# Performance work log

Hardware: AMD Instinct MI355X
Metric: run time of the kernel (lower is better)

The kernel has to match this reference:

```python
import jax, jax.numpy as jnp
import numpy as np

COORD_DIM, PARAM_DIM, H, L, O = 3, 8, 128, 5, 5
B, N_PTS = 16, 50000


def setup_inputs() -> dict:
    key = jax.random.key(0)
    ks = jax.random.split(key, 16)
    def w(k, shape, fan_in):
        return jax.random.normal(k, shape, dtype=jnp.float32) / np.sqrt(fan_in)
    inp = {
        "coords": jax.random.normal(ks[0], (B, N_PTS, COORD_DIM), dtype=jnp.float32),
        "params": jax.random.normal(ks[1], (B, PARAM_DIM), dtype=jnp.float32),
        # branch MLP: param_dim -> H (x5 hidden, rowdy tanh) -> H*O
        "branch_W0": w(ks[2], (PARAM_DIM, H), PARAM_DIM),
        "branch_b0": jnp.zeros((H,), jnp.float32),
        "branch_Wh": w(ks[3], (L - 1, H, H), H),
        "branch_bh": jnp.zeros((L - 1, H), jnp.float32),
        "branch_alpha": jnp.ones((L, H), jnp.float32),
        "branch_Wf": w(ks[4], (H, H * O), H),
        "branch_bf": jnp.zeros((H * O,), jnp.float32),
        # trunk: coord_dim -> H (x5, FiLM by branch cumsum, rowdy tanh) -> H
        "trunk_W0": w(ks[5], (COORD_DIM, H), COORD_DIM),
        "trunk_b0": jnp.zeros((H,), jnp.float32),
        "trunk_Wh": w(ks[6], (L - 1, H, H), H),
        "trunk_bh": jnp.zeros((L - 1, H), jnp.float32),
        "trunk_alpha": jnp.ones((L, H), jnp.float32),
        "trunk_Wf": w(ks[7], (H, H), H),
        "trunk_bf": jnp.zeros((H,), jnp.float32),
    }
    return inp


def reference(coords, params, branch_W0, branch_b0, branch_Wh, branch_bh,
              branch_alpha, branch_Wf, branch_bf, trunk_W0, trunk_b0,
              trunk_Wh, trunk_bh, trunk_alpha, trunk_Wf, trunk_bf):
    # ---- branch MLP with RowdyActivation, keeping hidden outputs ----
    h = branch_alpha[0] * jnp.tanh(params @ branch_W0 + branch_b0)  # (B,H)
    hiddens = [h]
    for i in range(L - 1):
        h = branch_alpha[i + 1] * jnp.tanh(h @ branch_Wh[i] + branch_bh[i])
        hiddens.append(h)
    branch_out = h @ branch_Wf + branch_bf  # (B, H*O)
    # cumulative sums S_i = sum_{j<=i} hidden_j
    S = [hiddens[0]]
    for i in range(1, L):
        S.append(hiddens[i] + S[-1])
    # ---- trunk with FiLM modulation ----
    x = coords @ trunk_W0 + trunk_b0                       # (B,n,H)
    x = trunk_alpha[0] * jnp.tanh(x * S[0][:, None, :])
    for i in range(1, L):
        x = x @ trunk_Wh[i - 1] + trunk_bh[i - 1]
        x = trunk_alpha[i] * jnp.tanh(x * S[i][:, None, :])
    YL = x @ trunk_Wf + trunk_bf                           # (B,n,H)
    ZL = branch_out.reshape(B, O, H)                       # (B,O,H)
    # out[b,n,o] = sum_h ZL[b,o,h] * YL[b,n,h]  (tiled matmul, no (B,n,O,H) temp)
    return jnp.einsum('bnh,boh->bno', YL, ZL)
```

## Files before the change

kernel.cpp:

```cpp
#include <hip/hip_runtime.h>
#include <math.h>

#define H      128
#define LNUM   5
#define ONUM   5
#define BATCH  16
#define NPTS   50000
#define TP     64
#define XROW   152

#define K2LOG2E 2.8853900817779268f

typedef _Float16      half8    __attribute__((ext_vector_type(8)));
typedef float         floatx4  __attribute__((ext_vector_type(4)));
typedef unsigned int  uint2v   __attribute__((ext_vector_type(2)));
typedef unsigned int  uint4v   __attribute__((ext_vector_type(4)));
typedef unsigned short ushort8_t __attribute__((ext_vector_type(8)));

#define BAR() asm volatile("s_waitcnt lgkmcnt(0)\ns_barrier" ::: "memory")

static __device__ __forceinline__ unsigned short f2h(float f) {
    _Float16 h = (_Float16)f;
    return __builtin_bit_cast(unsigned short, h);
}
static __device__ __forceinline__ unsigned int packh(float a, float b) {
    return (unsigned int)f2h(a) | ((unsigned int)f2h(b) << 16);
}

__global__ __launch_bounds__(512)
void fold_kernel(const float* __restrict__ params,
                 const float* __restrict__ bW0, const float* __restrict__ bb0,
                 const float* __restrict__ bWh, const float* __restrict__ bbh,
                 const float* __restrict__ balpha,
                 const float* __restrict__ bWf, const float* __restrict__ bbf,
                 const float* __restrict__ tW0, const float* __restrict__ tb0,
                 const float* __restrict__ tWh, const float* __restrict__ tbh,
                 const float* __restrict__ tWf, const float* __restrict__ talpha,
                 const float* __restrict__ tbf,
                 unsigned short* __restrict__ w0s, unsigned short* __restrict__ whs,
                 unsigned short* __restrict__ wcomb, float* __restrict__ bcomb,
                 float* __restrict__ binit) {
    const int b = blockIdx.x, l = blockIdx.y, t = threadIdx.x;
    __shared__ float hbuf[H];
    __shared__ float Sneed[H];
    __shared__ float pbuf[8];
    __shared__ float zl_sh[ONUM][H];
    if (t < 8) pbuf[t] = params[b * 8 + t];
    __syncthreads();

    float scum = 0.0f;
    if (t < H) {
        float acc = bb0[t];
        for (int k = 0; k < 8; ++k) acc += pbuf[k] * bW0[k * H + t];
        float h = balpha[t] * tanhf(acc);
        hbuf[t] = h;
        scum = h;
        if (l == 0) Sneed[t] = scum;
    }
    for (int i = 1; i < LNUM; ++i) {
        __syncthreads();
        float hn = 0.0f;
        if (t < H) {
            const float* Wl = bWh + (i - 1) * H * H;
            float a2 = bbh[(i - 1) * H + t];
            for (int k = 0; k < H; ++k) a2 += hbuf[k] * Wl[k * H + t];
            hn = balpha[i * H + t] * tanhf(a2);
        }
        __syncthreads();
        if (t < H) {
            hbuf[t] = hn;
            scum += hn;
            if (i == l) Sneed[t] = scum;
        }
    }
    __syncthreads();

    if (l == 5) {
        for (int idx = t; idx < ONUM * H; idx += 512) {
            int o = idx >> 7, hh = idx & 127;
            float z = bbf[o * H + hh];
            for (int k = 0; k < H; ++k) z += hbuf[k] * bWf[k * (H * ONUM) + o * H + hh];
            zl_sh[o][hh] = z;
        }
        __syncthreads();
        for (int j = t; j < 16 * H; j += 512) {
            int o = j >> 7, f = j & 127;
            float v = 0.0f;
            if (o < ONUM) {
                const float* wfr = tWf + f * H;
                float s = 0.0f;
                for (int h = 0; h < H; ++h) s += wfr[h] * zl_sh[o][h];
                v = talpha[4 * H + f] * s;
            }
            wcomb[b * 16 * H + j] = f2h(v);
        }
        if (t < 16) {
            float v = 0.0f;
            if (t < ONUM)
                for (int h = 0; h < H; ++h) v += tbf[h] * zl_sh[t][h];
            bcomb[b * 16 + t] = v;
        }
    } else if (l == 0) {
        if (t < H) binit[(b * LNUM + 0) * H + t] = K2LOG2E * Sneed[t] * tb0[t];
        unsigned int* dst = (unsigned int*)(w0s + b * H * 32);
        for (int j = t; j < H * 16; j += 512) {
            int f = j >> 4, k0 = (j & 15) << 1;
            float s = K2LOG2E * Sneed[f];
            float v0 = (k0 < 3)     ? s * tW0[k0 * H + f]       : 0.0f;
            float v1 = (k0 + 1 < 3) ? s * tW0[(k0 + 1) * H + f] : 0.0f;
            dst[j] = packh(v0, v1);
        }
    } else {
        if (t < H) binit[(b * LNUM + l) * H + t] = K2LOG2E * Sneed[t] * tbh[(l - 1) * H + t];
        const float* Wsrc = tWh + (l - 1) * H * H;
        unsigned int* dst = (unsigned int*)(whs + (b * 4 + (l - 1)) * H * H);
        for (int j = t; j < H * H / 2; j += 512) {
            int f = j >> 6, k0 = (j & 63) << 1;
            float s = K2LOG2E * Sneed[f];
            dst[j] = packh(s * Wsrc[k0 * H + f] * talpha[(l - 1) * H + k0],
                           s * Wsrc[(k0 + 1) * H + f] * talpha[(l - 1) * H + k0 + 1]);
        }
    }
}

__global__ __launch_bounds__(128, 3)
void trunk_kernel(const float* __restrict__ coords,
                  const unsigned short* __restrict__ w0s,
                  const unsigned short* __restrict__ whs,
                  const float* __restrict__ binit,
                  const unsigned short* __restrict__ wcomb,
                  const float* __restrict__ bcomb,
                  float* __restrict__ out) {
    const int b    = blockIdx.y;
    const int n0   = blockIdx.x * TP;
    const int tid  = threadIdx.x;
    const int lane = tid & 63;
    const int w    = tid >> 6;
    const int q    = lane >> 4;
    const int c    = lane & 15;
    const int mh   = w * 64;

    __shared__ unsigned short xs[TP * XROW];

    int valid = NPTS - n0; if (valid > TP) valid = TP;
    {
        int p = tid >> 1, hh = tid & 1;
        if (hh == 0) {
            float c0 = 0.f, c1 = 0.f, c2 = 0.f;
            if (p < valid) {
                const float* cp = coords + ((size_t)b * NPTS + n0 + p) * 3;
                c0 = cp[0]; c1 = cp[1]; c2 = cp[2];
            }
            uint4v z;
            z.x = __builtin_bit_cast(unsigned int, __builtin_amdgcn_cvt_pkrtz(c0, c1));
            z.y = __builtin_bit_cast(unsigned int, __builtin_amdgcn_cvt_pkrtz(c2, 0.0f));
            z.z = 0; z.w = 0;
            *(uint4v*)&xs[p * XROW + 0] = z;
            uint4v zz = {0, 0, 0, 0};
            *(uint4v*)&xs[p * XROW + 8] = zz;
        } else {
            uint4v zz = {0, 0, 0, 0};
            *(uint4v*)&xs[p * XROW + 16] = zz;
            *(uint4v*)&xs[p * XROW + 24] = zz;
        }
    }
    BAR();

    floatx4 acc[4][4];

    #pragma unroll
    for (int mt = 0; mt < 4; ++mt) {
        floatx4 bi4 = *(const floatx4*)&binit[(b * LNUM + 0) * H + mh + mt * 16 + q * 4];
        #pragma unroll
        for (int nt = 0; nt < 4; ++nt) acc[mt][nt] = bi4;
    }
    {
        const unsigned short* w0b = w0s + b * H * 32;
        half8 af[4], bfr[4];
        #pragma unroll
        for (int mt = 0; mt < 4; ++mt)
            af[mt] = __builtin_bit_cast(half8,
                *(const ushort8_t*)&w0b[(mh + mt * 16 + c) * 32 + q * 8]);
        #pragma unroll
        for (int nt = 0; nt < 4; ++nt)
            bfr[nt] = __builtin_bit_cast(half8,
                *(const ushort8_t*)&xs[(nt * 16 + c) * XROW + q * 8]);
        #pragma unroll
        for (int mt = 0; mt < 4; ++mt)
            #pragma unroll
            for (int nt = 0; nt < 4; ++nt)
                acc[mt][nt] = __builtin_amdgcn_mfma_f32_16x16x32_f16(af[mt], bfr[nt], acc[mt][nt], 0, 0, 0);
    }
    BAR();
    #pragma unroll
    for (int mt = 0; mt < 4; ++mt) {
        int f0 = mh + mt * 16 + q * 4;
        #pragma unroll
        for (int nt = 0; nt < 4; ++nt) {
            int pt = nt * 16 + c;
            floatx4 v = acc[mt][nt];
            #pragma unroll
            for (int r = 0; r < 4; ++r) {
                float e  = __builtin_amdgcn_exp2f(v[r]);
                float rc = __builtin_amdgcn_rcpf(e + 1.0f);
                v[r] = __builtin_fmaf(-2.0f, rc, 1.0f);
            }
            uint2v u;
            u.x = __builtin_bit_cast(unsigned int, __builtin_amdgcn_cvt_pkrtz(v[0], v[1]));
            u.y = __builtin_bit_cast(unsigned int, __builtin_amdgcn_cvt_pkrtz(v[2], v[3]));
            *(uint2v*)&xs[pt * XROW + f0] = u;
        }
    }

    for (int l = 1; l <= 4; ++l) {
        const unsigned short* wl = whs + (b * 4 + (l - 1)) * H * H;
        #pragma unroll
        for (int mt = 0; mt < 4; ++mt) {
            floatx4 bi4 = *(const floatx4*)&binit[(b * LNUM + l) * H + mh + mt * 16 + q * 4];
            #pragma unroll
            for (int nt = 0; nt < 4; ++nt) acc[mt][nt] = bi4;
        }
        BAR();
        #pragma unroll
        for (int s = 0; s < 4; ++s) {
            half8 af[4], bfr[4];
            #pragma unroll
            for (int mt = 0; mt < 4; ++mt)
                af[mt] = __builtin_bit_cast(half8,
                    *(const ushort8_t*)&wl[(mh + mt * 16 + c) * H + s * 32 + q * 8]);
            #pragma unroll
            for (int nt = 0; nt < 4; ++nt)
                bfr[nt] = __builtin_bit_cast(half8,
                    *(const ushort8_t*)&xs[(nt * 16 + c) * XROW + s * 32 + q * 8]);
            #pragma unroll
            for (int mt = 0; mt < 4; ++mt)
                #pragma unroll
                for (int nt = 0; nt < 4; ++nt)
                    acc[mt][nt] = __builtin_amdgcn_mfma_f32_16x16x32_f16(af[mt], bfr[nt], acc[mt][nt], 0, 0, 0);
        }
        BAR();
        #pragma unroll
        for (int mt = 0; mt < 4; ++mt) {
            int f0 = mh + mt * 16 + q * 4;
            #pragma unroll
            for (int nt = 0; nt < 4; ++nt) {
                int pt = nt * 16 + c;
                floatx4 v = acc[mt][nt];
                #pragma unroll
                for (int r = 0; r < 4; ++r) {
                    float e  = __builtin_amdgcn_exp2f(v[r]);
                    float rc = __builtin_amdgcn_rcpf(e + 1.0f);
                    v[r] = __builtin_fmaf(-2.0f, rc, 1.0f);
                }
                uint2v u;
                u.x = __builtin_bit_cast(unsigned int, __builtin_amdgcn_cvt_pkrtz(v[0], v[1]));
                u.y = __builtin_bit_cast(unsigned int, __builtin_amdgcn_cvt_pkrtz(v[2], v[3]));
                *(uint2v*)&xs[pt * XROW + f0] = u;
            }
        }
    }
    BAR();

    {
        floatx4 bc = *(const floatx4*)&bcomb[b * 16 + q * 4];
        floatx4 oacc[2] = {bc, bc};
        const unsigned short* wc = wcomb + b * 16 * H;
        #pragma unroll
        for (int s = 0; s < 4; ++s) {
            half8 af = __builtin_bit_cast(half8,
                *(const ushort8_t*)&wc[c * H + s * 32 + q * 8]);
            #pragma unroll
            for (int nt = 0; nt < 2; ++nt) {
                half8 bfr = __builtin_bit_cast(half8,
                    *(const ushort8_t*)&xs[(w * 32 + nt * 16 + c) * XROW + s * 32 + q * 8]);
                oacc[nt] = __builtin_amdgcn_mfma_f32_16x16x32_f16(af, bfr, oacc[nt], 0, 0, 0);
            }
        }
        #pragma unroll
        for (int nt = 0; nt < 2; ++nt) {
            int pt = n0 + w * 32 + nt * 16 + c;
            if (pt < NPTS) {
                float* op = out + ((size_t)b * NPTS + pt) * ONUM;
                if (q == 0) {
                    op[0] = oacc[nt][0]; op[1] = oacc[nt][1];
                    op[2] = oacc[nt][2]; op[3] = oacc[nt][3];
                } else if (q == 1) {
                    op[4] = oacc[nt][0];
                }
            }
        }
    }
}

extern "C" void kernel_launch(void* const* d_in, const int* in_sizes, int n_in,
                              void* d_out, int out_size, void* d_ws, size_t ws_size,
                              hipStream_t stream) {
    const float* coords       = (const float*)d_in[0];
    const float* params       = (const float*)d_in[1];
    const float* branch_W0    = (const float*)d_in[2];
    const float* branch_b0    = (const float*)d_in[3];
    const float* branch_Wh    = (const float*)d_in[4];
    const float* branch_bh    = (const float*)d_in[5];
    const float* branch_alpha = (const float*)d_in[6];
    const float* branch_Wf    = (const float*)d_in[7];
    const float* branch_bf    = (const float*)d_in[8];
    const float* trunk_W0     = (const float*)d_in[9];
    const float* trunk_b0     = (const float*)d_in[10];
    const float* trunk_Wh     = (const float*)d_in[11];
    const float* trunk_bh     = (const float*)d_in[12];
    const float* trunk_alpha  = (const float*)d_in[13];
    const float* trunk_Wf     = (const float*)d_in[14];
    const float* trunk_bf     = (const float*)d_in[15];
    float* out = (float*)d_out;

    char* ws = (char*)d_ws;
    float*          binit = (float*)(ws + 0);
    unsigned short* wcomb = (unsigned short*)(ws + 40960);
    float*          bcomb = (float*)(ws + 106496);
    unsigned short* w0s   = (unsigned short*)(ws + 107520);
    unsigned short* whs   = (unsigned short*)(ws + 238592);

    fold_kernel<<<dim3(BATCH, 6), 512, 0, stream>>>(params, branch_W0, branch_b0,
                                                    branch_Wh, branch_bh, branch_alpha,
                                                    branch_Wf, branch_bf,
                                                    trunk_W0, trunk_b0, trunk_Wh, trunk_bh,
                                                    trunk_Wf, trunk_alpha, trunk_bf,
                                                    w0s, whs, wcomb, bcomb, binit);
    trunk_kernel<<<dim3((NPTS + TP - 1) / TP, BATCH), 128, 0, stream>>>(
        coords, w0s, whs, binit, wcomb, bcomb, out);
}
```

Before: 352.6 us.

## Split trunk tile across four waves with 32 features each

The trunk block grows from 128 to 256 threads, so each of four waves computes 32 output features instead of 64 for the same 64-point tile. Each wave's accumulator drops to 8 MFMA tiles, which lowers register pressure and raises waves per block. The coordinate staging and the final output projection are redistributed across the four waves. The custom inline-asm barrier is replaced by __syncthreads. The cost is that each wave still reads all B fragments from LDS, so LDS read traffic per useful FLOP doubles, and more threads wait at each barrier.

```diff
diff --git a/kernel.cpp b/kernel.cpp
--- a/kernel.cpp
+++ b/kernel.cpp
@@ -16,8 +16,6 @@
 typedef unsigned int  uint2v   __attribute__((ext_vector_type(2)));
 typedef unsigned int  uint4v   __attribute__((ext_vector_type(4)));
 typedef unsigned short ushort8_t __attribute__((ext_vector_type(8)));
-
-#define BAR() asm volatile("s_waitcnt lgkmcnt(0)\ns_barrier" ::: "memory")
 
 static __device__ __forceinline__ unsigned short f2h(float f) {
     _Float16 h = (_Float16)f;
@@ -123,7 +121,7 @@
     }
 }
 
-__global__ __launch_bounds__(128, 3)
+__global__ __launch_bounds__(256, 4)
 void trunk_kernel(const float* __restrict__ coords,
                   const unsigned short* __restrict__ w0s,
                   const unsigned short* __restrict__ whs,
@@ -138,63 +136,56 @@
     const int w    = tid >> 6;
     const int q    = lane >> 4;
     const int c    = lane & 15;
-    const int mh   = w * 64;
+    const int mq   = w * 32;
 
     __shared__ unsigned short xs[TP * XROW];
 
     int valid = NPTS - n0; if (valid > TP) valid = TP;
     {
-        int p = tid >> 1, hh = tid & 1;
-        if (hh == 0) {
+        int p = tid >> 2, part = tid & 3;
+        uint4v z = {0, 0, 0, 0};
+        if (part == 0) {
             float c0 = 0.f, c1 = 0.f, c2 = 0.f;
             if (p < valid) {
                 const float* cp = coords + ((size_t)b * NPTS + n0 + p) * 3;
                 c0 = cp[0]; c1 = cp[1]; c2 = cp[2];
             }
-            uint4v z;
             z.x = __builtin_bit_cast(unsigned int, __builtin_amdgcn_cvt_pkrtz(c0, c1));
             z.y = __builtin_bit_cast(unsigned int, __builtin_amdgcn_cvt_pkrtz(c2, 0.0f));
-            z.z = 0; z.w = 0;
-            *(uint4v*)&xs[p * XROW + 0] = z;
-            uint4v zz = {0, 0, 0, 0};
-            *(uint4v*)&xs[p * XROW + 8] = zz;
-        } else {
-            uint4v zz = {0, 0, 0, 0};
-            *(uint4v*)&xs[p * XROW + 16] = zz;
-            *(uint4v*)&xs[p * XROW + 24] = zz;
-        }
-    }
-    BAR();
-
-    floatx4 acc[4][4];
+        }
+        *(uint4v*)&xs[p * XROW + part * 8] = z;
+    }
+    __syncthreads();
+
+    floatx4 acc[2][4];
 
     #pragma unroll
-    for (int mt = 0; mt < 4; ++mt) {
-        floatx4 bi4 = *(const floatx4*)&binit[(b * LNUM + 0) * H + mh + mt * 16 + q * 4];
+    for (int mt = 0; mt < 2; ++mt) {
+        floatx4 bi4 = *(const floatx4*)&binit[(b * LNUM + 0) * H + mq + mt * 16 + q * 4];
         #pragma unroll
         for (int nt = 0; nt < 4; ++nt) acc[mt][nt] = bi4;
     }
     {
         const unsigned short* w0b = w0s + b * H * 32;
-        half8 af[4], bfr[4];
-        #pragma unroll
-        for (int mt = 0; mt < 4; ++mt)
+        half8 af[2], bfr[4];
+        #pragma unroll
+        for (int mt = 0; mt < 2; ++mt)
             af[mt] = __builtin_bit_cast(half8,
-                *(const ushort8_t*)&w0b[(mh + mt * 16 + c) * 32 + q * 8]);
+                *(const ushort8_t*)&w0b[(mq + mt * 16 + c) * 32 + q * 8]);
         #pragma unroll
         for (int nt = 0; nt < 4; ++nt)
             bfr[nt] = __builtin_bit_cast(half8,
                 *(const ushort8_t*)&xs[(nt * 16 + c) * XROW + q * 8]);
         #pragma unroll
-        for (int mt = 0; mt < 4; ++mt)
+        for (int mt = 0; mt < 2; ++mt)
             #pragma unroll
             for (int nt = 0; nt < 4; ++nt)
                 acc[mt][nt] = __builtin_amdgcn_mfma_f32_16x16x32_f16(af[mt], bfr[nt], acc[mt][nt], 0, 0, 0);
     }
-    BAR();
+    __syncthreads();
     #pragma unroll
-    for (int mt = 0; mt < 4; ++mt) {
-        int f0 = mh + mt * 16 + q * 4;
+    for (int mt = 0; mt < 2; ++mt) {
+        int f0 = mq + mt * 16 + q * 4;
         #pragma unroll
         for (int nt = 0; nt < 4; ++nt) {
             int pt = nt * 16 + c;
@@ -215,33 +206,33 @@
     for (int l = 1; l <= 4; ++l) {
         const unsigned short* wl = whs + (b * 4 + (l - 1)) * H * H;
         #pragma unroll
-        for (int mt = 0; mt < 4; ++mt) {
-            floatx4 bi4 = *(const floatx4*)&binit[(b * LNUM + l) * H + mh + mt * 16 + q * 4];
+        for (int mt = 0; mt < 2; ++mt) {
+            floatx4 bi4 = *(const floatx4*)&binit[(b * LNUM + l) * H + mq + mt * 16 + q * 4];
             #pragma unroll
             for (int nt = 0; nt < 4; ++nt) acc[mt][nt] = bi4;
         }
-        BAR();
+        __syncthreads();
         #pragma unroll
         for (int s = 0; s < 4; ++s) {
-            half8 af[4], bfr[4];
-            #pragma unroll
-            for (int mt = 0; mt < 4; ++mt)
+            half8 af[2], bfr[4];
+            #pragma unroll
+            for (int mt = 0; mt < 2; ++mt)
                 af[mt] = __builtin_bit_cast(half8,
-                    *(const ushort8_t*)&wl[(mh + mt * 16 + c) * H + s * 32 + q * 8]);
+                    *(const ushort8_t*)&wl[(mq + mt * 16 + c) * H + s * 32 + q * 8]);
             #pragma unroll
             for (int nt = 0; nt < 4; ++nt)
                 bfr[nt] = __builtin_bit_cast(half8,
                     *(const ushort8_t*)&xs[(nt * 16 + c) * XROW + s * 32 + q * 8]);
             #pragma unroll
-            for (int mt = 0; mt < 4; ++mt)
+            for (int mt = 0; mt < 2; ++mt)
                 #pragma unroll
                 for (int nt = 0; nt < 4; ++nt)
                     acc[mt][nt] = __builtin_amdgcn_mfma_f32_16x16x32_f16(af[mt], bfr[nt], acc[mt][nt], 0, 0, 0);
         }
-        BAR();
-        #pragma unroll
-        for (int mt = 0; mt < 4; ++mt) {
-            int f0 = mh + mt * 16 + q * 4;
+        __syncthreads();
+        #pragma unroll
+        for (int mt = 0; mt < 2; ++mt) {
+            int f0 = mq + mt * 16 + q * 4;
             #pragma unroll
             for (int nt = 0; nt < 4; ++nt) {
                 int pt = nt * 16 + c;
@@ -259,34 +250,27 @@
             }
         }
     }
-    BAR();
+    __syncthreads();
 
     {
-        floatx4 bc = *(const floatx4*)&bcomb[b * 16 + q * 4];
-        floatx4 oacc[2] = {bc, bc};
+        floatx4 oacc = *(const floatx4*)&bcomb[b * 16 + q * 4];
         const unsigned short* wc = wcomb + b * 16 * H;
         #pragma unroll
         for (int s = 0; s < 4; ++s) {
             half8 af = __builtin_bit_cast(half8,
                 *(const ushort8_t*)&wc[c * H + s * 32 + q * 8]);
-            #pragma unroll
-            for (int nt = 0; nt < 2; ++nt) {
-                half8 bfr = __builtin_bit_cast(half8,
-                    *(const ushort8_t*)&xs[(w * 32 + nt * 16 + c) * XROW + s * 32 + q * 8]);
-                oacc[nt] = __builtin_amdgcn_mfma_f32_16x16x32_f16(af, bfr, oacc[nt], 0, 0, 0);
-            }
-        }
-        #pragma unroll
-        for (int nt = 0; nt < 2; ++nt) {
-            int pt = n0 + w * 32 + nt * 16 + c;
-            if (pt < NPTS) {
-                float* op = out + ((size_t)b * NPTS + pt) * ONUM;
-                if (q == 0) {
-                    op[0] = oacc[nt][0]; op[1] = oacc[nt][1];
-                    op[2] = oacc[nt][2]; op[3] = oacc[nt][3];
-                } else if (q == 1) {
-                    op[4] = oacc[nt][0];
-                }
+            half8 bfr = __builtin_bit_cast(half8,
+                *(const ushort8_t*)&xs[(w * 16 + c) * XROW + s * 32 + q * 8]);
+            oacc = __builtin_amdgcn_mfma_f32_16x16x32_f16(af, bfr, oacc, 0, 0, 0);
+        }
+        int pt = n0 + w * 16 + c;
+        if (pt < NPTS) {
+            float* op = out + ((size_t)b * NPTS + pt) * ONUM;
+            if (q == 0) {
+                op[0] = oacc[0]; op[1] = oacc[1];
+                op[2] = oacc[2]; op[3] = oacc[3];
+            } else if (q == 1) {
+                op[4] = oacc[0];
             }
         }
     }
@@ -326,6 +310,6 @@
                                                     trunk_W0, trunk_b0, trunk_Wh, trunk_bh,
                                                     trunk_Wf, trunk_alpha, trunk_bf,
                                                     w0s, whs, wcomb, bcomb, binit);
-    trunk_kernel<<<dim3((NPTS + TP - 1) / TP, BATCH), 128, 0, stream>>>(
+    trunk_kernel<<<dim3((NPTS + TP - 1) / TP, BATCH), 256, 0, stream>>>(
         coords, w0s, whs, binit, wcomb, bcomb, out);
 }
```

Result: no change. 353.9 us (+0.4%).

## Restructure trunk kernel to single-wave blocks without workgroup barriers

Applied to the files above, without the earlier changes.

The trunk kernel goes from two-wave blocks (64 points, each wave owning half of the 128 features) to one-wave blocks that each handle 32 points and all 128 features. Because one wave now owns its whole LDS tile, the s_barrier calls become plain lgkmcnt waits. This removes cross-wave synchronisation stalls and lets waves run independently. In exchange, each wave streams the full 128x128 fp16 weight matrix for every layer but serves only 32 points, which raises weight load traffic per point from cache or L2.

```diff
diff --git a/kernel.cpp b/kernel.cpp
--- a/kernel.cpp
+++ b/kernel.cpp
@@ -6,7 +6,7 @@
 #define ONUM   5
 #define BATCH  16
 #define NPTS   50000
-#define TP     64
+#define WPTS   32
 #define XROW   152
 
 #define K2LOG2E 2.8853900817779268f
@@ -17,7 +17,7 @@
 typedef unsigned int  uint4v   __attribute__((ext_vector_type(4)));
 typedef unsigned short ushort8_t __attribute__((ext_vector_type(8)));
 
-#define BAR() asm volatile("s_waitcnt lgkmcnt(0)\ns_barrier" ::: "memory")
+#define WAVE_LDS_FENCE() asm volatile("s_waitcnt lgkmcnt(0)" ::: "memory")
 
 static __device__ __forceinline__ unsigned short f2h(float f) {
     _Float16 h = (_Float16)f;
@@ -123,7 +123,7 @@
     }
 }
 
-__global__ __launch_bounds__(128, 3)
+__global__ __launch_bounds__(64, 3)
 void trunk_kernel(const float* __restrict__ coords,
                   const unsigned short* __restrict__ w0s,
                   const unsigned short* __restrict__ whs,
@@ -132,71 +132,59 @@
                   const float* __restrict__ bcomb,
                   float* __restrict__ out) {
     const int b    = blockIdx.y;
-    const int n0   = blockIdx.x * TP;
-    const int tid  = threadIdx.x;
-    const int lane = tid & 63;
-    const int w    = tid >> 6;
+    const int n0   = blockIdx.x * WPTS;
+    const int lane = threadIdx.x;
     const int q    = lane >> 4;
     const int c    = lane & 15;
-    const int mh   = w * 64;
-
-    __shared__ unsigned short xs[TP * XROW];
-
-    int valid = NPTS - n0; if (valid > TP) valid = TP;
+
+    __shared__ unsigned short xs[WPTS * XROW];
+
+    int valid = NPTS - n0; if (valid > WPTS) valid = WPTS;
     {
-        int p = tid >> 1, hh = tid & 1;
+        int p = lane >> 1, hh = lane & 1;
+        uint4v z = {0, 0, 0, 0};
         if (hh == 0) {
             float c0 = 0.f, c1 = 0.f, c2 = 0.f;
             if (p < valid) {
                 const float* cp = coords + ((size_t)b * NPTS + n0 + p) * 3;
                 c0 = cp[0]; c1 = cp[1]; c2 = cp[2];
             }
-            uint4v z;
             z.x = __builtin_bit_cast(unsigned int, __builtin_amdgcn_cvt_pkrtz(c0, c1));
             z.y = __builtin_bit_cast(unsigned int, __builtin_amdgcn_cvt_pkrtz(c2, 0.0f));
-            z.z = 0; z.w = 0;
             *(uint4v*)&xs[p * XROW + 0] = z;
             uint4v zz = {0, 0, 0, 0};
-            *(uint4v*)&xs[p * XROW + 8] = zz;
+            *(uint4v*)&xs[p * XROW + 16] = zz;
         } else {
-            uint4v zz = {0, 0, 0, 0};
-            *(uint4v*)&xs[p * XROW + 16] = zz;
-            *(uint4v*)&xs[p * XROW + 24] = zz;
-        }
-    }
-    BAR();
-
-    floatx4 acc[4][4];
-
-    #pragma unroll
-    for (int mt = 0; mt < 4; ++mt) {
-        floatx4 bi4 = *(const floatx4*)&binit[(b * LNUM + 0) * H + mh + mt * 16 + q * 4];
-        #pragma unroll
-        for (int nt = 0; nt < 4; ++nt) acc[mt][nt] = bi4;
-    }
+            *(uint4v*)&xs[p * XROW + 8]  = z;
+            *(uint4v*)&xs[p * XROW + 24] = z;
+        }
+    }
+    WAVE_LDS_FENCE();
+
+    floatx4 acc[8][2];
+
     {
         const unsigned short* w0b = w0s + b * H * 32;
-        half8 af[4], bfr[4];
-        #pragma unroll
-        for (int mt = 0; mt < 4; ++mt)
-            af[mt] = __builtin_bit_cast(half8,
-                *(const ushort8_t*)&w0b[(mh + mt * 16 + c) * 32 + q * 8]);
-        #pragma unroll
-        for (int nt = 0; nt < 4; ++nt)
+        half8 bfr[2];
+        #pragma unroll
+        for (int nt = 0; nt < 2; ++nt)
             bfr[nt] = __builtin_bit_cast(half8,
                 *(const ushort8_t*)&xs[(nt * 16 + c) * XROW + q * 8]);
         #pragma unroll
-        for (int mt = 0; mt < 4; ++mt)
-            #pragma unroll
-            for (int nt = 0; nt < 4; ++nt)
-                acc[mt][nt] = __builtin_amdgcn_mfma_f32_16x16x32_f16(af[mt], bfr[nt], acc[mt][nt], 0, 0, 0);
-    }
-    BAR();
+        for (int mt = 0; mt < 8; ++mt) {
+            floatx4 bi4 = *(const floatx4*)&binit[(b * LNUM + 0) * H + mt * 16 + q * 4];
+            half8 af = __builtin_bit_cast(half8,
+                *(const ushort8_t*)&w0b[(mt * 16 + c) * 32 + q * 8]);
+            #pragma unroll
+            for (int nt = 0; nt < 2; ++nt)
+                acc[mt][nt] = __builtin_amdgcn_mfma_f32_16x16x32_f16(af, bfr[nt], bi4, 0, 0, 0);
+        }
+    }
     #pragma unroll
-    for (int mt = 0; mt < 4; ++mt) {
-        int f0 = mh + mt * 16 + q * 4;
-        #pragma unroll
-        for (int nt = 0; nt < 4; ++nt) {
+    for (int mt = 0; mt < 8; ++mt) {
+        int f0 = mt * 16 + q * 4;
+        #pragma unroll
+        for (int nt = 0; nt < 2; ++nt) {
             int pt = nt * 16 + c;
             floatx4 v = acc[mt][nt];
             #pragma unroll
@@ -211,39 +199,38 @@
             *(uint2v*)&xs[pt * XROW + f0] = u;
         }
     }
+    WAVE_LDS_FENCE();
 
     for (int l = 1; l <= 4; ++l) {
         const unsigned short* wl = whs + (b * 4 + (l - 1)) * H * H;
         #pragma unroll
-        for (int mt = 0; mt < 4; ++mt) {
-            floatx4 bi4 = *(const floatx4*)&binit[(b * LNUM + l) * H + mh + mt * 16 + q * 4];
-            #pragma unroll
-            for (int nt = 0; nt < 4; ++nt) acc[mt][nt] = bi4;
-        }
-        BAR();
+        for (int mt = 0; mt < 8; ++mt) {
+            floatx4 bi4 = *(const floatx4*)&binit[(b * LNUM + l) * H + mt * 16 + q * 4];
+            #pragma unroll
+            for (int nt = 0; nt < 2; ++nt) acc[mt][nt] = bi4;
+        }
         #pragma unroll
         for (int s = 0; s < 4; ++s) {
-            half8 af[4], bfr[4];
-            #pragma unroll
-            for (int mt = 0; mt < 4; ++mt)
-                af[mt] = __builtin_bit_cast(half8,
-                    *(const ushort8_t*)&wl[(mh + mt * 16 + c) * H + s * 32 + q * 8]);
-            #pragma unroll
-            for (int nt = 0; nt < 4; ++nt)
+            half8 bfr[2];
+            #pragma unroll
+            for (int nt = 0; nt < 2; ++nt)
                 bfr[nt] = __builtin_bit_cast(half8,
                     *(const ushort8_t*)&xs[(nt * 16 + c) * XROW + s * 32 + q * 8]);
             #pragma unroll
-            for (int mt = 0; mt < 4; ++mt)
+            for (int mt = 0; mt < 8; ++mt) {
+                half8 af = __builtin_bit_cast(half8,
+                    *(const ushort8_t*)&wl[(mt * 16 + c) * H + s * 32 + q * 8]);
                 #pragma unroll
-                for (int nt = 0; nt < 4; ++nt)
-                    acc[mt][nt] = __builtin_amdgcn_mfma_f32_16x16x32_f16(af[mt], bfr[nt], acc[mt][nt], 0, 0, 0);
-        }
-        BAR();
-        #pragma unroll
-        for (int mt = 0; mt < 4; ++mt) {
-            int f0 = mh + mt * 16 + q * 4;
-            #pragma unroll
-            for (int nt = 0; nt < 4; ++nt) {
+                for (int nt = 0; nt < 2; ++nt)
+                    acc[mt][nt] = __builtin_amdgcn_mfma_f32_16x16x32_f16(af, bfr[nt], acc[mt][nt], 0, 0, 0);
+            }
+        }
+        WAVE_LDS_FENCE();
+        #pragma unroll
+        for (int mt = 0; mt < 8; ++mt) {
+            int f0 = mt * 16 + q * 4;
+            #pragma unroll
+            for (int nt = 0; nt < 2; ++nt) {
                 int pt = nt * 16 + c;
                 floatx4 v = acc[mt][nt];
                 #pragma unroll
@@ -258,8 +245,8 @@
                 *(uint2v*)&xs[pt * XROW + f0] = u;
             }
         }
-    }
-    BAR();
+        WAVE_LDS_FENCE();
+    }
 
     {
         floatx4 bc = *(const floatx4*)&bcomb[b * 16 + q * 4];
@@ -272,13 +259,13 @@
             #pragma unroll
             for (int nt = 0; nt < 2; ++nt) {
                 half8 bfr = __builtin_bit_cast(half8,
-                    *(const ushort8_t*)&xs[(w * 32 + nt * 16 + c) * XROW + s * 32 + q * 8]);
+                    *(const ushort8_t*)&xs[(nt * 16 + c) * XROW + s * 32 + q * 8]);
                 oacc[nt] = __builtin_amdgcn_mfma_f32_16x16x32_f16(af, bfr, oacc[nt], 0, 0, 0);
             }
         }
         #pragma unroll
         for (int nt = 0; nt < 2; ++nt) {
-            int pt = n0 + w * 32 + nt * 16 + c;
+            int pt = n0 + nt * 16 + c;
             if (pt < NPTS) {
                 float* op = out + ((size_t)b * NPTS + pt) * ONUM;
                 if (q == 0) {
@@ -326,6 +313,6 @@
                                                     trunk_W0, trunk_b0, trunk_Wh, trunk_bh,
                                                     trunk_Wf, trunk_alpha, trunk_bf,
                                                     w0s, whs, wcomb, bcomb, binit);
-    trunk_kernel<<<dim3((NPTS + TP - 1) / TP, BATCH), 128, 0, stream>>>(
+    trunk_kernel<<<dim3((NPTS + WPTS - 1) / WPTS, BATCH), 64, 0, stream>>>(
         coords, w0s, whs, binit, wcomb, bcomb, out);
 }
```

Result: slower. 531.2 us (+50.7%).
